# Performance work log

Hardware: AMD Instinct MI355X
Metric: run time of the kernel (lower is better)

The kernel has to match this reference:

```python
import jax, jax.numpy as jnp
import numpy as np

B, N, L, D, H, NLAYERS, V = 8, 1024, 16, 256, 4, 2, 32000
DH = D // H  # per-head dim


def setup_inputs() -> dict:
    key = jax.random.key(0)
    ks = jax.random.split(key, 7)
    cfg_adj = jax.random.randint(ks[0], (B, N, N), 0, 2, dtype=jnp.int32)
    cfg_nodes = jax.random.randint(ks[1], (B, N, L), 0, V, dtype=jnp.int32)
    cfg_len = jax.random.randint(ks[2], (B,), 1, N + 1, dtype=jnp.int32)
    emb = jax.random.normal(ks[3], (V, D), jnp.float32) * 0.02
    # xavier-ish scale for per-head projections and attention vectors
    W = jax.random.normal(ks[4], (NLAYERS, H, D, DH), jnp.float32) * np.float32(np.sqrt(2.0 / (D + DH)))
    a_src = jax.random.normal(ks[5], (NLAYERS, H, DH), jnp.float32) * 0.1
    a_dst = jax.random.normal(ks[6], (NLAYERS, H, DH), jnp.float32) * 0.1
    ln_scale = jnp.ones((NLAYERS, D), jnp.float32)
    ln_bias = jnp.zeros((NLAYERS, D), jnp.float32)
    return {"cfg_adj": cfg_adj, "cfg_nodes": cfg_nodes, "cfg_len": cfg_len,
            "emb": emb, "W": W, "a_src": a_src, "a_dst": a_dst,
            "ln_scale": ln_scale, "ln_bias": ln_bias}


def _layer_norm(x, scale, bias, eps=1e-5):
    mu = jnp.mean(x, axis=-1, keepdims=True)
    var = jnp.var(x, axis=-1, keepdims=True)
    return (x - mu) * jax.lax.rsqrt(var + eps) * scale + bias


def reference(cfg_adj, cfg_nodes, cfg_len, emb, W, a_src, a_dst, ln_scale, ln_bias):
    # node features: mean over token embeddings (dropout is identity in eval)
    node_feat = emb[cfg_nodes].mean(axis=2)                       # (B,N,D)
    # add self-loops once (repeated add+clamp in the original is idempotent)
    adj = jnp.minimum(cfg_adj + jnp.eye(N, dtype=cfg_adj.dtype)[None], 1)
    neg_mask = (adj == 0)[:, None]                                # (B,1,N,N)
    h = node_feat
    for l in range(NLAYERS):
        Wh = jnp.einsum('bnd,hdk->bhnk', h, W[l])                 # (B,H,N,DH)
        src = jnp.einsum('bhnk,hk->bhn', Wh, a_src[l])            # (B,H,N)
        dst = jnp.einsum('bhnk,hk->bhn', Wh, a_dst[l])            # (B,H,N)
        e = jax.nn.leaky_relu(src[:, :, :, None] + dst[:, :, None, :], 0.2)
        e = jnp.where(neg_mask, jnp.float32(-1e9), e)             # masked fill
        alpha = jax.nn.softmax(e, axis=-1)                        # (B,H,N,N)
        h_prime = jnp.einsum('bhnm,bhmk->bhnk', alpha, Wh)        # (B,H,N,DH)
        h_cat = jnp.transpose(h_prime, (0, 2, 1, 3)).reshape(B, N, D)
        h = _layer_norm(h + h_cat, ln_scale[l], ln_bias[l])
    return h, cfg_len
```

## Files before the change

kernel.cpp:

```cpp
#include <hip/hip_runtime.h>
#include <math.h>

#define B 8
#define N 1024
#define L 16
#define D 256
#define H 4
#define DH 64
#define NLAYERS 2
#define V 32000

typedef __attribute__((ext_vector_type(8))) short short8;
typedef __attribute__((ext_vector_type(4))) float f32x4;

union U8 { uint4 u; short8 s; };

__device__ inline unsigned short f2bf(float x) {
    unsigned u = __float_as_uint(x);
    u = (u + 0x7fff + ((u >> 16) & 1)) >> 16;
    return (unsigned short)u;
}
__device__ inline float bf2f(unsigned short x) {
    return __uint_as_float(((unsigned)x) << 16);
}


#define PACK_BLK 2048
#define WT_BLK   (NLAYERS * H * 4)
#define FEAT_BLK 2048
#define PRE1_GRID (PACK_BLK + WT_BLK + FEAT_BLK + 1)

__global__ __launch_bounds__(256) void k_pre1(const int* __restrict__ adj,
                                              const float* __restrict__ W,
                                              const int* __restrict__ len,
                                              const float* __restrict__ emb,
                                              const int* __restrict__ nodes,
                                              unsigned long long* __restrict__ pack,
                                              unsigned short* __restrict__ WT_sw,
                                              unsigned short* __restrict__ h_sw,
                                              float* __restrict__ out_len) {
    int bid = blockIdx.x;
    int t = threadIdx.x;
    if (bid < PACK_BLK) {
        int row = bid * 4 + (t >> 6);
        int lane = t & 63;
        int n = row & (N - 1);
        const int* arow = adj + (long)row * N;
        unsigned long long* prow = pack + (size_t)row * 16;
        int g16 = lane & 15;
#pragma unroll
        for (int it = 0; it < 4; ++it) {
            int m0 = it * 256 + lane * 4;
            int4 a = *(const int4*)(arow + m0);
            unsigned nib = (unsigned)((a.x != 0) || (m0 == n))
                         | ((unsigned)((a.y != 0) || (m0 + 1 == n)) << 1)
                         | ((unsigned)((a.z != 0) || (m0 + 2 == n)) << 2)
                         | ((unsigned)((a.w != 0) || (m0 + 3 == n)) << 3);
            unsigned long long v = (unsigned long long)nib << (g16 * 4);
            v |= __shfl_xor(v, 1, 64);
            v |= __shfl_xor(v, 2, 64);
            v |= __shfl_xor(v, 4, 64);
            v |= __shfl_xor(v, 8, 64);
            if (g16 == 0) prow[it * 4 + (lane >> 4)] = v;
        }
    } else if (bid < PACK_BLK + WT_BLK) {
        int idx = bid - PACK_BLK;
        int lh = idx >> 2, q = idx & 3;
        const float* Wl = W + (size_t)lh * D * DH;
        int dh = t & 63;
        int d0 = q * 64 + (t >> 6) * 16;
#pragma unroll
        for (int i = 0; i < 16; ++i) {
            int d = d0 + i;
            WT_sw[(((size_t)lh * 8 + (d >> 5)) * 64 + dh) * 32 + (d & 31)] = f2bf(Wl[(size_t)d * DH + dh]);
        }
    } else if (bid < PACK_BLK + WT_BLK + FEAT_BLK) {
        int row = (bid - PACK_BLK - WT_BLK) * 4 + (t >> 6);
        int lane = t & 63;
        int d4 = lane * 4;
        const int* np = nodes + row * L;
        float4 s = make_float4(0.f, 0.f, 0.f, 0.f);
#pragma unroll
        for (int l = 0; l < L; ++l) {
            float4 v = *(const float4*)&emb[(size_t)np[l] * D + d4];
            s.x += v.x; s.y += v.y; s.z += v.z; s.w += v.w;
        }
        s.x *= (1.0f / L); s.y *= (1.0f / L); s.z *= (1.0f / L); s.w *= (1.0f / L);
        int b = row >> 10, n = row & 1023;
        ushort4 o;
        o.x = f2bf(s.x); o.y = f2bf(s.y); o.z = f2bf(s.z); o.w = f2bf(s.w);
        *(ushort4*)&h_sw[(((size_t)b * 64 + (n >> 4)) * 8 + (d4 >> 5)) * 512 + (n & 15) * 32 + (d4 & 31)] = o;
    } else {
        if (t < B) out_len[t] = (float)len[t];
    }
}

__global__ __launch_bounds__(256) void k_wh(const unsigned short* __restrict__ h_sw,
                                            const unsigned short* __restrict__ WT_l,
                                            const float* __restrict__ asrc_l,
                                            const float* __restrict__ adst_l,
                                            unsigned short* __restrict__ WhT,
                                            float* __restrict__ srcv,
                                            float* __restrict__ dstv) {
    __shared__ float red[4][16][68];
    int bt = blockIdx.x;
    int hh = blockIdx.y;
    int b = bt >> 6;
    int nt = bt & 63;
    int n0 = nt * 16;
    int tid = threadIdx.x;
    int w = tid >> 6, lane = tid & 63;
    int rowLane = lane & 15, quad = lane >> 4;
    int bh = b * H + hh;
    const unsigned short* abase = h_sw + (((size_t)b * 64 + nt) * 8) * 512 + rowLane * 32 + quad * 8;
    const unsigned short* bbase = WT_l + ((size_t)hh * 8) * 2048 + rowLane * 32 + quad * 8;
    f32x4 acc[4] = {};
#pragma unroll
    for (int kk = 0; kk < 2; ++kk) {
        int kc = w * 2 + kk;
        short8 af = *(const short8*)(abase + kc * 512);
#pragma unroll
        for (int c = 0; c < 4; ++c) {
            short8 bf = *(const short8*)(bbase + kc * 2048 + c * 512);
            acc[c] = __builtin_amdgcn_mfma_f32_16x16x32_bf16(af, bf, acc[c], 0, 0, 0);
        }
    }
#pragma unroll
    for (int c = 0; c < 4; ++c)
#pragma unroll
        for (int r = 0; r < 4; ++r)
            red[w][quad * 4 + r][c * 16 + rowLane] = acc[c][r];
    __syncthreads();
    int dh = tid >> 2, j4 = tid & 3;
    float v[4];
#pragma unroll
    for (int i = 0; i < 4; ++i)
        v[i] = red[0][j4 * 4 + i][dh] + red[1][j4 * 4 + i][dh] + red[2][j4 * 4 + i][dh] + red[3][j4 * 4 + i][dh];
    ushort4 o;
    o.x = f2bf(v[0]); o.y = f2bf(v[1]); o.z = f2bf(v[2]); o.w = f2bf(v[3]);
    *(ushort4*)&WhT[(((size_t)bh * 32 + (n0 >> 5)) * 64 + dh) * 32 + (n0 & 31) + j4 * 4] = o;
    float as = asrc_l[hh * DH + dh];
    float ad = adst_l[hh * DH + dh];
    float* ps = &red[0][0][0];
    float* pd = ps + 16 * 68;
    __syncthreads();
#pragma unroll
    for (int i = 0; i < 4; ++i) {
        ps[(j4 * 4 + i) * 68 + dh] = v[i] * as;
        pd[(j4 * 4 + i) * 68 + dh] = v[i] * ad;
    }
    __syncthreads();
    int nl = tid >> 4, g = tid & 15;
    float4 s4 = *(float4*)&ps[nl * 68 + g * 4];
    float4 t4 = *(float4*)&pd[nl * 68 + g * 4];
    float s1 = s4.x + s4.y + s4.z + s4.w;
    float d1 = t4.x + t4.y + t4.z + t4.w;
#pragma unroll
    for (int off = 8; off; off >>= 1) {
        s1 += __shfl_xor(s1, off, 16);
        d1 += __shfl_xor(d1, off, 16);
    }
    if (g == 0) {
        srcv[bh * N + n0 + nl] = s1;
        dstv[bh * N + n0 + nl] = d1;
    }
}

__global__ __launch_bounds__(256) void k_attn(const unsigned long long* __restrict__ pack,
                                              const float* __restrict__ srcv,
                                              const float* __restrict__ dstv,
                                              const unsigned short* __restrict__ WhT,
                                              unsigned short* __restrict__ hp_bf) {
    __shared__ float red[4][16][68];
    __shared__ float ssum[4][16];
    float* dsts = &red[0][0][0];

    int tid = threadIdx.x;
    int bt = blockIdx.x;
    int bh = bt >> 6;
    int n0 = (bt & 63) * 16;
    int b = bh >> 2;
    int w = tid >> 6, lane = tid & 63;
    int rowLane = lane & 15, quad = lane >> 4;
    int n = n0 + rowLane;

    {
        float4 v = *(const float4*)(dstv + bh * N + w * 256 + lane * 4);
        *(float4*)(dsts + w * 256 + lane * 4) = v;
    }
    const uint4* pbp = (const uint4*)((const unsigned char*)(pack + ((size_t)(b * N + n)) * 16) + w * 32);
    uint4 pbv0 = pbp[0];
    uint4 pbv1 = pbp[1];
    float src = srcv[bh * N + n];
    float mx = src > 0.f ? src : 0.2f * src;

    unsigned words[8] = {pbv0.x, pbv0.y, pbv0.z, pbv0.w, pbv1.x, pbv1.y, pbv1.z, pbv1.w};
    const unsigned short* wbase = WhT + ((size_t)bh * 32) * 2048 + rowLane * 32 + quad * 8;
    f32x4 acc[4] = {};
    float sum0 = 0.f, sum1 = 0.f;
#pragma unroll
    for (int t2 = 0; t2 < 8; ++t2) {
        unsigned bits = (words[t2] >> (quad * 8)) & 0xffu;
        float4 d0 = *(const float4*)(dsts + w * 256 + t2 * 32 + quad * 8);
        float4 d1 = *(const float4*)(dsts + w * 256 + t2 * 32 + quad * 8 + 4);
        float dd[8] = {d0.x, d0.y, d0.z, d0.w, d1.x, d1.y, d1.z, d1.w};
        unsigned pk[4];
#pragma unroll
        for (int j2 = 0; j2 < 4; ++j2) {
            float ea = src + dd[2 * j2];
            float eb = src + dd[2 * j2 + 1];
            ea = ea > 0.f ? ea : 0.2f * ea;
            eb = eb > 0.f ? eb : 0.2f * eb;
            float pa = ((bits >> (2 * j2)) & 1) ? __expf(ea - mx) : 0.f;
            float pb = ((bits >> (2 * j2 + 1)) & 1) ? __expf(eb - mx) : 0.f;
            sum0 += pa; sum1 += pb;
            pk[j2] = (__float_as_uint(pb) & 0xffff0000u) | (__float_as_uint(pa) >> 16);
        }
        U8 u; u.u = make_uint4(pk[0], pk[1], pk[2], pk[3]);
        short8 af = u.s;
        const unsigned short* tb = wbase + (size_t)(w * 8 + t2) * 2048;
        acc[0] = __builtin_amdgcn_mfma_f32_16x16x32_bf16(af, *(const short8*)(tb + 0 * 512), acc[0], 0, 0, 0);
        acc[1] = __builtin_amdgcn_mfma_f32_16x16x32_bf16(af, *(const short8*)(tb + 1 * 512), acc[1], 0, 0, 0);
        acc[2] = __builtin_amdgcn_mfma_f32_16x16x32_bf16(af, *(const short8*)(tb + 2 * 512), acc[2], 0, 0, 0);
        acc[3] = __builtin_amdgcn_mfma_f32_16x16x32_bf16(af, *(const short8*)(tb + 3 * 512), acc[3], 0, 0, 0);
    }
    float sum = sum0 + sum1;
    sum += __shfl_xor(sum, 16, 64);
    sum += __shfl_xor(sum, 32, 64);
    if (quad == 0) ssum[w][rowLane] = sum;
    __syncthreads();
#pragma unroll
    for (int c = 0; c < 4; ++c)
#pragma unroll
        for (int r = 0; r < 4; ++r)
            red[w][quad * 4 + r][c * 16 + rowLane] = acc[c][r];
    __syncthreads();
    int row = tid >> 4, col4 = (tid & 15) * 4;
    float4 s = make_float4(0.f, 0.f, 0.f, 0.f);
#pragma unroll
    for (int ww = 0; ww < 4; ++ww) {
        float4 v = *(const float4*)&red[ww][row][col4];
        s.x += v.x; s.y += v.y; s.z += v.z; s.w += v.w;
    }
    float invr = 1.0f / (ssum[0][row] + ssum[1][row] + ssum[2][row] + ssum[3][row]);
    ushort4 o;
    o.x = f2bf(s.x * invr); o.y = f2bf(s.y * invr);
    o.z = f2bf(s.z * invr); o.w = f2bf(s.w * invr);
    *(ushort4*)&hp_bf[((size_t)bh * N + n0 + row) * DH + col4] = o;
}

__global__ __launch_bounds__(256) void k_ln(const unsigned short* __restrict__ h_sw_in,
                                            const unsigned short* __restrict__ hp_bf,
                                            const float* __restrict__ scale,
                                            const float* __restrict__ bias,
                                            float* __restrict__ out,
                                            unsigned short* __restrict__ h_sw_out,
                                            int layer, int is_final) {
    __shared__ float red[8];
    int bn = blockIdx.x;
    int b = bn >> 10, n = bn & 1023;
    int c = threadIdx.x;
    int hh = c >> 6, k = c & 63;
    size_t swidx = (((size_t)b * 64 + (n >> 4)) * 8 + (c >> 5)) * 512 + (n & 15) * 32 + (c & 31);
    float x = bf2f(h_sw_in[swidx]) + bf2f(hp_bf[((size_t)(b * H + hh) * N + n) * DH + k]);
    float s = x, s2 = x * x;
#pragma unroll
    for (int off = 32; off; off >>= 1) {
        s += __shfl_xor(s, off, 64);
        s2 += __shfl_xor(s2, off, 64);
    }
    int w = c >> 6, lane = c & 63;
    if (lane == 0) { red[w] = s; red[4 + w] = s2; }
    __syncthreads();
    s = red[0] + red[1] + red[2] + red[3];
    s2 = red[4] + red[5] + red[6] + red[7];
    float mu = s * (1.0f / D);
    float var = s2 * (1.0f / D) - mu * mu;
    float r = rsqrtf(var + 1e-5f);
    float y = (x - mu) * r * scale[layer * D + c] + bias[layer * D + c];
    if (is_final) out[(size_t)bn * D + c] = y;
    else h_sw_out[swidx] = f2bf(y);
}

extern "C" void kernel_launch(void* const* d_in, const int* in_sizes, int n_in,
                              void* d_out, int out_size, void* d_ws, size_t ws_size,
                              hipStream_t stream) {
    const int* cfg_adj = (const int*)d_in[0];
    const int* cfg_nodes = (const int*)d_in[1];
    const int* cfg_len = (const int*)d_in[2];
    const float* emb = (const float*)d_in[3];
    const float* W = (const float*)d_in[4];
    const float* a_src = (const float*)d_in[5];
    const float* a_dst = (const float*)d_in[6];
    const float* ln_scale = (const float*)d_in[7];
    const float* ln_bias = (const float*)d_in[8];
    float* out = (float*)d_out;
    float* ws = (float*)d_ws;

    float* srcv = ws;
    float* dstv = srcv + (size_t)B * H * N;
    unsigned short* h_sw = (unsigned short*)(dstv + (size_t)B * H * N);
    unsigned short* WhT = h_sw + (size_t)B * N * D;
    unsigned short* WT_sw = WhT + (size_t)B * H * DH * N;
    unsigned short* hp_bf = WT_sw + (size_t)NLAYERS * H * DH * D;
    unsigned long long* pack = (unsigned long long*)(hp_bf + (size_t)B * H * N * DH);

    k_pre1<<<PRE1_GRID, 256, 0, stream>>>(cfg_adj, W, cfg_len, emb, cfg_nodes,
                                          pack, WT_sw, h_sw, out + (size_t)B * N * D);
    for (int l = 0; l < NLAYERS; ++l) {
        k_wh<<<dim3(B * 64, H), 256, 0, stream>>>(
            h_sw, WT_sw + (size_t)l * H * 8 * 2048,
            a_src + (size_t)l * H * DH, a_dst + (size_t)l * H * DH,
            WhT, srcv, dstv);
        k_attn<<<B * H * 64, 256, 0, stream>>>(pack, srcv, dstv, WhT, hp_bf);
        k_ln<<<B * N, 256, 0, stream>>>(h_sw, hp_bf, ln_scale, ln_bias,
                                        out, h_sw, l, l == NLAYERS - 1 ? 1 : 0);
    }
}
```

Baseline: 197.4 us.

## Fuse feature gather, projection, attention and layernorm into per-tile kernels

Moves the embedding-mean into a new kernel that also computes the layer-0 Wh projection and the src/dst scores per 16-node tile. The attention kernel now processes all four heads of a 16-row tile in one block, with each wave covering the full N range for one head. It then does the residual layernorm in-block and computes the next layer's projection from the normalized tile, so the separate k_wh and k_ln launches and the hp_bf round trip are gone. It double-buffers the WhT fragment loads, stages pack bits and dst scores in LDS, and ping-pongs WhT/srcv/dstv buffers between layers. The cost is 4x fewer blocks for attention (512 instead of 2048), which may reduce occupancy and latency hiding, and each wave now does a 32-step serial loop.

```diff
diff --git a/kernel.cpp b/kernel.cpp
--- a/kernel.cpp
+++ b/kernel.cpp
@@ -27,18 +27,14 @@
 
 #define PACK_BLK 2048
 #define WT_BLK   (NLAYERS * H * 4)
-#define FEAT_BLK 2048
-#define PRE1_GRID (PACK_BLK + WT_BLK + FEAT_BLK + 1)
-
-__global__ __launch_bounds__(256) void k_pre1(const int* __restrict__ adj,
-                                              const float* __restrict__ W,
-                                              const int* __restrict__ len,
-                                              const float* __restrict__ emb,
-                                              const int* __restrict__ nodes,
-                                              unsigned long long* __restrict__ pack,
-                                              unsigned short* __restrict__ WT_sw,
-                                              unsigned short* __restrict__ h_sw,
-                                              float* __restrict__ out_len) {
+#define PRE_GRID (PACK_BLK + WT_BLK + 1)
+
+__global__ __launch_bounds__(256) void k_pre(const int* __restrict__ adj,
+                                             const float* __restrict__ W,
+                                             const int* __restrict__ len,
+                                             unsigned long long* __restrict__ pack,
+                                             unsigned short* __restrict__ WT_sw,
+                                             float* __restrict__ out_len) {
     int bid = blockIdx.x;
     int t = threadIdx.x;
     if (bid < PACK_BLK) {
@@ -74,135 +70,157 @@
             int d = d0 + i;
             WT_sw[(((size_t)lh * 8 + (d >> 5)) * 64 + dh) * 32 + (d & 31)] = f2bf(Wl[(size_t)d * DH + dh]);
         }
-    } else if (bid < PACK_BLK + WT_BLK + FEAT_BLK) {
-        int row = (bid - PACK_BLK - WT_BLK) * 4 + (t >> 6);
-        int lane = t & 63;
-        int d4 = lane * 4;
-        const int* np = nodes + row * L;
-        float4 s = make_float4(0.f, 0.f, 0.f, 0.f);
-#pragma unroll
-        for (int l = 0; l < L; ++l) {
-            float4 v = *(const float4*)&emb[(size_t)np[l] * D + d4];
-            s.x += v.x; s.y += v.y; s.z += v.z; s.w += v.w;
-        }
-        s.x *= (1.0f / L); s.y *= (1.0f / L); s.z *= (1.0f / L); s.w *= (1.0f / L);
-        int b = row >> 10, n = row & 1023;
-        ushort4 o;
-        o.x = f2bf(s.x); o.y = f2bf(s.y); o.z = f2bf(s.z); o.w = f2bf(s.w);
-        *(ushort4*)&h_sw[(((size_t)b * 64 + (n >> 4)) * 8 + (d4 >> 5)) * 512 + (n & 15) * 32 + (d4 & 31)] = o;
     } else {
         if (t < B) out_len[t] = (float)len[t];
     }
 }
 
-__global__ __launch_bounds__(256) void k_wh(const unsigned short* __restrict__ h_sw,
-                                            const unsigned short* __restrict__ WT_l,
-                                            const float* __restrict__ asrc_l,
-                                            const float* __restrict__ adst_l,
-                                            unsigned short* __restrict__ WhT,
-                                            float* __restrict__ srcv,
-                                            float* __restrict__ dstv) {
-    __shared__ float red[4][16][68];
+__device__ inline void wh_tile(const unsigned short* __restrict__ hA,
+                               const unsigned short* __restrict__ WT_l,
+                               const float* __restrict__ asrc_l,
+                               const float* __restrict__ adst_l,
+                               unsigned short* __restrict__ WhT_out,
+                               float* __restrict__ srcv_out,
+                               float* __restrict__ dstv_out,
+                               int b, int n0, int hh, int lane) {
+    int rowLane = lane & 15, quad = lane >> 4;
+    int bh = b * H + hh;
+    const unsigned short* abase = hA + rowLane * 32 + quad * 8;
+    const unsigned short* bbase = WT_l + (size_t)hh * 16384 + rowLane * 32 + quad * 8;
+    f32x4 acc[4] = {};
+#pragma unroll
+    for (int kc = 0; kc < 8; ++kc) {
+        short8 af = *(const short8*)(abase + kc * 512);
+#pragma unroll
+        for (int c = 0; c < 4; ++c) {
+            short8 bf = *(const short8*)(bbase + (size_t)kc * 2048 + c * 512);
+            acc[c] = __builtin_amdgcn_mfma_f32_16x16x32_bf16(af, bf, acc[c], 0, 0, 0);
+        }
+    }
+    int m0 = n0 + quad * 4;
+    float ps[4] = {0.f, 0.f, 0.f, 0.f}, pd[4] = {0.f, 0.f, 0.f, 0.f};
+#pragma unroll
+    for (int c = 0; c < 4; ++c) {
+        int dh = c * 16 + rowLane;
+        ushort4 o;
+        o.x = f2bf(acc[c][0]); o.y = f2bf(acc[c][1]);
+        o.z = f2bf(acc[c][2]); o.w = f2bf(acc[c][3]);
+        *(ushort4*)&WhT_out[(((size_t)bh * 32 + (m0 >> 5)) * 64 + dh) * 32 + (m0 & 31)] = o;
+        float as = asrc_l[hh * DH + dh];
+        float ad = adst_l[hh * DH + dh];
+#pragma unroll
+        for (int r = 0; r < 4; ++r) { ps[r] += acc[c][r] * as; pd[r] += acc[c][r] * ad; }
+    }
+#pragma unroll
+    for (int off = 1; off < 16; off <<= 1) {
+#pragma unroll
+        for (int r = 0; r < 4; ++r) {
+            ps[r] += __shfl_xor(ps[r], off, 64);
+            pd[r] += __shfl_xor(pd[r], off, 64);
+        }
+    }
+    if (rowLane == 0) {
+#pragma unroll
+        for (int r = 0; r < 4; ++r) {
+            srcv_out[bh * N + m0 + r] = ps[r];
+            dstv_out[bh * N + m0 + r] = pd[r];
+        }
+    }
+}
+
+__global__ __launch_bounds__(1024) void k_feat(const float* __restrict__ emb,
+                                               const int* __restrict__ nodes,
+                                               unsigned short* __restrict__ h_sw,
+                                               const unsigned short* __restrict__ WT0,
+                                               const float* __restrict__ asrc0,
+                                               const float* __restrict__ adst0,
+                                               unsigned short* __restrict__ WhT0,
+                                               float* __restrict__ srcv0,
+                                               float* __restrict__ dstv0) {
+    __shared__ __align__(16) int nodesLds[256];
+    __shared__ __align__(16) unsigned short hA[8 * 16 * 32];
+    int tid = threadIdx.x;
     int bt = blockIdx.x;
-    int hh = blockIdx.y;
-    int b = bt >> 6;
-    int nt = bt & 63;
-    int n0 = nt * 16;
+    int b = bt >> 6, nt = bt & 63, n0 = nt * 16;
+    if (tid < 256) nodesLds[tid] = nodes[(size_t)(b * N + n0) * L + tid];
+    __syncthreads();
+    int w = tid >> 6, lane = tid & 63;
+    int d4 = lane * 4;
+    const int* np = nodesLds + w * L;
+    float4 s = make_float4(0.f, 0.f, 0.f, 0.f);
+#pragma unroll
+    for (int l = 0; l < L; ++l) {
+        float4 v = *(const float4*)&emb[(size_t)np[l] * D + d4];
+        s.x += v.x; s.y += v.y; s.z += v.z; s.w += v.w;
+    }
+    s.x *= (1.0f / L); s.y *= (1.0f / L); s.z *= (1.0f / L); s.w *= (1.0f / L);
+    ushort4 o;
+    o.x = f2bf(s.x); o.y = f2bf(s.y); o.z = f2bf(s.z); o.w = f2bf(s.w);
+    int off = (d4 >> 5) * 512 + w * 32 + (d4 & 31);
+    *(ushort4*)&hA[off] = o;
+    *(ushort4*)&h_sw[((size_t)(b * 64 + nt) * 8) * 512 + off] = o;
+    __syncthreads();
+    if (w < 4) wh_tile(hA, WT0, asrc0, adst0, WhT0, srcv0, dstv0, b, n0, w, lane);
+}
+
+template <int FINAL>
+__global__ __launch_bounds__(256) void k_attn_f(const unsigned long long* __restrict__ pack,
+                                                const float* __restrict__ srcv_in,
+                                                const float* __restrict__ dstv_in,
+                                                const unsigned short* __restrict__ WhT_in,
+                                                unsigned short* __restrict__ h_sw,
+                                                const float* __restrict__ scale_l,
+                                                const float* __restrict__ bias_l,
+                                                const unsigned short* __restrict__ WT_next,
+                                                const float* __restrict__ asrc_n,
+                                                const float* __restrict__ adst_n,
+                                                unsigned short* __restrict__ WhT_out,
+                                                float* __restrict__ srcv_out,
+                                                float* __restrict__ dstv_out,
+                                                float* __restrict__ out) {
+    __shared__ __align__(16) char smem[25600];
+    float* dsts = (float*)smem;
+    unsigned long long* packs = (unsigned long long*)(smem + 16384);
+    float* xt = (float*)smem;
+    unsigned short* hA = (unsigned short*)(smem + 17408);
+
     int tid = threadIdx.x;
+    int bt = blockIdx.x;
+    int b = bt >> 6, nt = bt & 63, n0 = nt * 16;
     int w = tid >> 6, lane = tid & 63;
     int rowLane = lane & 15, quad = lane >> 4;
-    int bh = b * H + hh;
-    const unsigned short* abase = h_sw + (((size_t)b * 64 + nt) * 8) * 512 + rowLane * 32 + quad * 8;
-    const unsigned short* bbase = WT_l + ((size_t)hh * 8) * 2048 + rowLane * 32 + quad * 8;
-    f32x4 acc[4] = {};
-#pragma unroll
-    for (int kk = 0; kk < 2; ++kk) {
-        int kc = w * 2 + kk;
-        short8 af = *(const short8*)(abase + kc * 512);
-#pragma unroll
-        for (int c = 0; c < 4; ++c) {
-            short8 bf = *(const short8*)(bbase + kc * 2048 + c * 512);
-            acc[c] = __builtin_amdgcn_mfma_f32_16x16x32_bf16(af, bf, acc[c], 0, 0, 0);
-        }
-    }
-#pragma unroll
-    for (int c = 0; c < 4; ++c)
-#pragma unroll
-        for (int r = 0; r < 4; ++r)
-            red[w][quad * 4 + r][c * 16 + rowLane] = acc[c][r];
-    __syncthreads();
-    int dh = tid >> 2, j4 = tid & 3;
-    float v[4];
-#pragma unroll
-    for (int i = 0; i < 4; ++i)
-        v[i] = red[0][j4 * 4 + i][dh] + red[1][j4 * 4 + i][dh] + red[2][j4 * 4 + i][dh] + red[3][j4 * 4 + i][dh];
-    ushort4 o;
-    o.x = f2bf(v[0]); o.y = f2bf(v[1]); o.z = f2bf(v[2]); o.w = f2bf(v[3]);
-    *(ushort4*)&WhT[(((size_t)bh * 32 + (n0 >> 5)) * 64 + dh) * 32 + (n0 & 31) + j4 * 4] = o;
-    float as = asrc_l[hh * DH + dh];
-    float ad = adst_l[hh * DH + dh];
-    float* ps = &red[0][0][0];
-    float* pd = ps + 16 * 68;
-    __syncthreads();
-#pragma unroll
-    for (int i = 0; i < 4; ++i) {
-        ps[(j4 * 4 + i) * 68 + dh] = v[i] * as;
-        pd[(j4 * 4 + i) * 68 + dh] = v[i] * ad;
-    }
-    __syncthreads();
-    int nl = tid >> 4, g = tid & 15;
-    float4 s4 = *(float4*)&ps[nl * 68 + g * 4];
-    float4 t4 = *(float4*)&pd[nl * 68 + g * 4];
-    float s1 = s4.x + s4.y + s4.z + s4.w;
-    float d1 = t4.x + t4.y + t4.z + t4.w;
-#pragma unroll
-    for (int off = 8; off; off >>= 1) {
-        s1 += __shfl_xor(s1, off, 16);
-        d1 += __shfl_xor(d1, off, 16);
-    }
-    if (g == 0) {
-        srcv[bh * N + n0 + nl] = s1;
-        dstv[bh * N + n0 + nl] = d1;
-    }
-}
-
-__global__ __launch_bounds__(256) void k_attn(const unsigned long long* __restrict__ pack,
-                                              const float* __restrict__ srcv,
-                                              const float* __restrict__ dstv,
-                                              const unsigned short* __restrict__ WhT,
-                                              unsigned short* __restrict__ hp_bf) {
-    __shared__ float red[4][16][68];
-    __shared__ float ssum[4][16];
-    float* dsts = &red[0][0][0];
-
-    int tid = threadIdx.x;
-    int bt = blockIdx.x;
-    int bh = bt >> 6;
-    int n0 = (bt & 63) * 16;
-    int b = bh >> 2;
-    int w = tid >> 6, lane = tid & 63;
-    int rowLane = lane & 15, quad = lane >> 4;
-    int n = n0 + rowLane;
+    int bh = b * H + w;
 
     {
-        float4 v = *(const float4*)(dstv + bh * N + w * 256 + lane * 4);
-        *(float4*)(dsts + w * 256 + lane * 4) = v;
-    }
-    const uint4* pbp = (const uint4*)((const unsigned char*)(pack + ((size_t)(b * N + n)) * 16) + w * 32);
-    uint4 pbv0 = pbp[0];
-    uint4 pbv1 = pbp[1];
-    float src = srcv[bh * N + n];
+        const float* dv = dstv_in + (size_t)bh * N;
+#pragma unroll
+        for (int k = 0; k < 4; ++k)
+            *(float4*)(dsts + w * 1024 + k * 256 + lane * 4) = *(const float4*)(dv + k * 256 + lane * 4);
+        packs[tid] = pack[((size_t)(b * N + n0 + (tid >> 4))) * 16 + (tid & 15)];
+    }
+    __syncthreads();
+
+    float src = srcv_in[bh * N + n0 + rowLane];
     float mx = src > 0.f ? src : 0.2f * src;
-
-    unsigned words[8] = {pbv0.x, pbv0.y, pbv0.z, pbv0.w, pbv1.x, pbv1.y, pbv1.z, pbv1.w};
-    const unsigned short* wbase = WhT + ((size_t)bh * 32) * 2048 + rowLane * 32 + quad * 8;
+    const unsigned* prow = (const unsigned*)packs + rowLane * 32;
+    const unsigned short* wbase = WhT_in + (size_t)bh * 65536 + rowLane * 32 + quad * 8;
+    const float* dw = dsts + w * 1024 + quad * 8;
+
     f32x4 acc[4] = {};
     float sum0 = 0.f, sum1 = 0.f;
-#pragma unroll
-    for (int t2 = 0; t2 < 8; ++t2) {
-        unsigned bits = (words[t2] >> (quad * 8)) & 0xffu;
-        float4 d0 = *(const float4*)(dsts + w * 256 + t2 * 32 + quad * 8);
-        float4 d1 = *(const float4*)(dsts + w * 256 + t2 * 32 + quad * 8 + 4);
+    short8 fb[2][4];
+#pragma unroll
+    for (int c = 0; c < 4; ++c) fb[0][c] = *(const short8*)(wbase + c * 512);
+#pragma unroll 2
+    for (int t2 = 0; t2 < 32; ++t2) {
+        int cb = t2 & 1;
+        int t2n = (t2 + 1) & 31;
+#pragma unroll
+        for (int c = 0; c < 4; ++c)
+            fb[cb ^ 1][c] = *(const short8*)(wbase + (size_t)t2n * 2048 + c * 512);
+        unsigned bits = (prow[t2] >> (quad * 8)) & 0xffu;
+        float4 d0 = *(const float4*)(dw + t2 * 32);
+        float4 d1 = *(const float4*)(dw + t2 * 32 + 4);
         float dd[8] = {d0.x, d0.y, d0.z, d0.w, d1.x, d1.y, d1.z, d1.w};
         unsigned pk[4];
 #pragma unroll
@@ -218,68 +236,82 @@
         }
         U8 u; u.u = make_uint4(pk[0], pk[1], pk[2], pk[3]);
         short8 af = u.s;
-        const unsigned short* tb = wbase + (size_t)(w * 8 + t2) * 2048;
-        acc[0] = __builtin_amdgcn_mfma_f32_16x16x32_bf16(af, *(const short8*)(tb + 0 * 512), acc[0], 0, 0, 0);
-        acc[1] = __builtin_amdgcn_mfma_f32_16x16x32_bf16(af, *(const short8*)(tb + 1 * 512), acc[1], 0, 0, 0);
-        acc[2] = __builtin_amdgcn_mfma_f32_16x16x32_bf16(af, *(const short8*)(tb + 2 * 512), acc[2], 0, 0, 0);
-        acc[3] = __builtin_amdgcn_mfma_f32_16x16x32_bf16(af, *(const short8*)(tb + 3 * 512), acc[3], 0, 0, 0);
+        acc[0] = __builtin_amdgcn_mfma_f32_16x16x32_bf16(af, fb[cb][0], acc[0], 0, 0, 0);
+        acc[1] = __builtin_amdgcn_mfma_f32_16x16x32_bf16(af, fb[cb][1], acc[1], 0, 0, 0);
+        acc[2] = __builtin_amdgcn_mfma_f32_16x16x32_bf16(af, fb[cb][2], acc[2], 0, 0, 0);
+        acc[3] = __builtin_amdgcn_mfma_f32_16x16x32_bf16(af, fb[cb][3], acc[3], 0, 0, 0);
     }
     float sum = sum0 + sum1;
     sum += __shfl_xor(sum, 16, 64);
     sum += __shfl_xor(sum, 32, 64);
-    if (quad == 0) ssum[w][rowLane] = sum;
+    float inv[4];
+#pragma unroll
+    for (int r = 0; r < 4; ++r) inv[r] = 1.0f / __shfl(sum, quad * 4 + r, 64);
+
     __syncthreads();
 #pragma unroll
     for (int c = 0; c < 4; ++c)
 #pragma unroll
         for (int r = 0; r < 4; ++r)
-            red[w][quad * 4 + r][c * 16 + rowLane] = acc[c][r];
-    __syncthreads();
-    int row = tid >> 4, col4 = (tid & 15) * 4;
-    float4 s = make_float4(0.f, 0.f, 0.f, 0.f);
-#pragma unroll
-    for (int ww = 0; ww < 4; ++ww) {
-        float4 v = *(const float4*)&red[ww][row][col4];
-        s.x += v.x; s.y += v.y; s.z += v.z; s.w += v.w;
-    }
-    float invr = 1.0f / (ssum[0][row] + ssum[1][row] + ssum[2][row] + ssum[3][row]);
-    ushort4 o;
-    o.x = f2bf(s.x * invr); o.y = f2bf(s.y * invr);
-    o.z = f2bf(s.z * invr); o.w = f2bf(s.w * invr);
-    *(ushort4*)&hp_bf[((size_t)bh * N + n0 + row) * DH + col4] = o;
-}
-
-__global__ __launch_bounds__(256) void k_ln(const unsigned short* __restrict__ h_sw_in,
-                                            const unsigned short* __restrict__ hp_bf,
-                                            const float* __restrict__ scale,
-                                            const float* __restrict__ bias,
-                                            float* __restrict__ out,
-                                            unsigned short* __restrict__ h_sw_out,
-                                            int layer, int is_final) {
-    __shared__ float red[8];
-    int bn = blockIdx.x;
-    int b = bn >> 10, n = bn & 1023;
-    int c = threadIdx.x;
-    int hh = c >> 6, k = c & 63;
-    size_t swidx = (((size_t)b * 64 + (n >> 4)) * 8 + (c >> 5)) * 512 + (n & 15) * 32 + (c & 31);
-    float x = bf2f(h_sw_in[swidx]) + bf2f(hp_bf[((size_t)(b * H + hh) * N + n) * DH + k]);
-    float s = x, s2 = x * x;
-#pragma unroll
-    for (int off = 32; off; off >>= 1) {
+            xt[(quad * 4 + r) * 268 + w * 64 + c * 16 + rowLane] = acc[c][r] * inv[r];
+    __syncthreads();
+
+    int row = tid >> 4, g = tid & 15;
+    size_t hsb = ((size_t)(b * 64 + nt) * 8 + (g >> 1)) * 512 + row * 32 + (g & 1) * 16;
+    U8 r0, r1;
+    r0.u = *(const uint4*)(h_sw + hsb);
+    r1.u = *(const uint4*)(h_sw + hsb + 8);
+    float4 xr[4];
+#pragma unroll
+    for (int k = 0; k < 4; ++k) xr[k] = *(const float4*)(xt + row * 268 + g * 16 + k * 4);
+    float xv[16];
+    float s = 0.f, s2 = 0.f;
+#pragma unroll
+    for (int j = 0; j < 16; ++j) {
+        unsigned short hv = (j < 8) ? ((const unsigned short*)&r0)[j] : ((const unsigned short*)&r1)[j - 8];
+        float x = bf2f(hv) + ((const float*)xr)[j];
+        xv[j] = x; s += x; s2 += x * x;
+    }
+#pragma unroll
+    for (int off = 1; off < 16; off <<= 1) {
         s += __shfl_xor(s, off, 64);
         s2 += __shfl_xor(s2, off, 64);
     }
-    int w = c >> 6, lane = c & 63;
-    if (lane == 0) { red[w] = s; red[4 + w] = s2; }
-    __syncthreads();
-    s = red[0] + red[1] + red[2] + red[3];
-    s2 = red[4] + red[5] + red[6] + red[7];
     float mu = s * (1.0f / D);
     float var = s2 * (1.0f / D) - mu * mu;
-    float r = rsqrtf(var + 1e-5f);
-    float y = (x - mu) * r * scale[layer * D + c] + bias[layer * D + c];
-    if (is_final) out[(size_t)bn * D + c] = y;
-    else h_sw_out[swidx] = f2bf(y);
+    float rstd = rsqrtf(var + 1e-5f);
+    int d0 = g * 16;
+    if (FINAL) {
+        float* orow = out + ((size_t)(b * N) + n0 + row) * D + d0;
+#pragma unroll
+        for (int k = 0; k < 4; ++k) {
+            float4 sc = *(const float4*)(scale_l + d0 + k * 4);
+            float4 bi = *(const float4*)(bias_l + d0 + k * 4);
+            float4 y;
+            y.x = (xv[k * 4 + 0] - mu) * rstd * sc.x + bi.x;
+            y.y = (xv[k * 4 + 1] - mu) * rstd * sc.y + bi.y;
+            y.z = (xv[k * 4 + 2] - mu) * rstd * sc.z + bi.z;
+            y.w = (xv[k * 4 + 3] - mu) * rstd * sc.w + bi.w;
+            *(float4*)(orow + k * 4) = y;
+        }
+    } else {
+        U8 o0, o1;
+#pragma unroll
+        for (int j = 0; j < 16; ++j) {
+            float scv = scale_l[d0 + j];
+            float biv = bias_l[d0 + j];
+            unsigned short yb = f2bf((xv[j] - mu) * rstd * scv + biv);
+            if (j < 8) ((unsigned short*)&o0)[j] = yb;
+            else ((unsigned short*)&o1)[j - 8] = yb;
+        }
+        *(uint4*)(h_sw + hsb) = o0.u;
+        *(uint4*)(h_sw + hsb + 8) = o1.u;
+        unsigned short* ha = hA + (g >> 1) * 512 + row * 32 + (g & 1) * 16;
+        *(uint4*)ha = o0.u;
+        *(uint4*)(ha + 8) = o1.u;
+        __syncthreads();
+        wh_tile(hA, WT_next, asrc_n, adst_n, WhT_out, srcv_out, dstv_out, b, n0, w, lane);
+    }
 }
 
 extern "C" void kernel_launch(void* const* d_in, const int* in_sizes, int n_in,
@@ -297,23 +329,26 @@
     float* out = (float*)d_out;
     float* ws = (float*)d_ws;
 
-    float* srcv = ws;
-    float* dstv = srcv + (size_t)B * H * N;
-    unsigned short* h_sw = (unsigned short*)(dstv + (size_t)B * H * N);
-    unsigned short* WhT = h_sw + (size_t)B * N * D;
-    unsigned short* WT_sw = WhT + (size_t)B * H * DH * N;
-    unsigned short* hp_bf = WT_sw + (size_t)NLAYERS * H * DH * D;
-    unsigned long long* pack = (unsigned long long*)(hp_bf + (size_t)B * H * N * DH);
-
-    k_pre1<<<PRE1_GRID, 256, 0, stream>>>(cfg_adj, W, cfg_len, emb, cfg_nodes,
-                                          pack, WT_sw, h_sw, out + (size_t)B * N * D);
-    for (int l = 0; l < NLAYERS; ++l) {
-        k_wh<<<dim3(B * 64, H), 256, 0, stream>>>(
-            h_sw, WT_sw + (size_t)l * H * 8 * 2048,
-            a_src + (size_t)l * H * DH, a_dst + (size_t)l * H * DH,
-            WhT, srcv, dstv);
-        k_attn<<<B * H * 64, 256, 0, stream>>>(pack, srcv, dstv, WhT, hp_bf);
-        k_ln<<<B * N, 256, 0, stream>>>(h_sw, hp_bf, ln_scale, ln_bias,
-                                        out, h_sw, l, l == NLAYERS - 1 ? 1 : 0);
-    }
-}
+    float* srcv0 = ws;
+    float* dstv0 = srcv0 + (size_t)B * H * N;
+    float* srcv1 = dstv0 + (size_t)B * H * N;
+    float* dstv1 = srcv1 + (size_t)B * H * N;
+    unsigned short* h_sw = (unsigned short*)(dstv1 + (size_t)B * H * N);
+    unsigned short* WhT0 = h_sw + (size_t)B * N * D;
+    unsigned short* WhT1 = WhT0 + (size_t)B * H * DH * N;
+    unsigned short* WT_sw = WhT1 + (size_t)B * H * DH * N;
+    unsigned long long* pack = (unsigned long long*)(WT_sw + (size_t)NLAYERS * H * DH * D);
+
+    k_pre<<<PRE_GRID, 256, 0, stream>>>(cfg_adj, W, cfg_len, pack, WT_sw, out + (size_t)B * N * D);
+    k_feat<<<B * 64, 1024, 0, stream>>>(emb, cfg_nodes, h_sw, WT_sw, a_src, a_dst,
+                                        WhT0, srcv0, dstv0);
+    k_attn_f<0><<<B * 64, 256, 0, stream>>>(pack, srcv0, dstv0, WhT0, h_sw,
+                                            ln_scale, ln_bias,
+                                            WT_sw + (size_t)H * DH * D,
+                                            a_src + (size_t)H * DH, a_dst + (size_t)H * DH,
+                                            WhT1, srcv1, dstv1, nullptr);
+    k_attn_f<1><<<B * 64, 256, 0, stream>>>(pack, srcv1, dstv1, WhT1, h_sw,
+                                            ln_scale + D, ln_bias + D,
+                                            nullptr, nullptr, nullptr,
+                                            nullptr, nullptr, nullptr, out);
+}
```

Measured after the change: 173.5 us. -12.1%, faster.
